# Kernel tuning notes

Hardware: AMD Instinct MI355X
Metric: run time of the kernel (lower is better)

## Reference

```python
import jax, jax.numpy as jnp
import numpy as np

N, M, D_IN, H1, D, OUT_C = 2048, 128, 352, 512, 256, 13


def _lin_bn_relu(x, w, b, g, be):
    # 1x1 conv == linear over last dim; BN (eval) folded to per-channel affine (g, be)
    return jax.nn.relu(g * (x @ w.T + b) + be)


def _encode(x, wA, bA, gA, beA, wB, bB, gB, beB):
    return _lin_bn_relu(_lin_bn_relu(x, wA, bA, gA, beA), wB, bB, gB, beB)


def setup_inputs() -> dict:
    key = jax.random.key(0)
    ks = iter(jax.random.split(key, 64))

    def wgt(shape, s=0.05):
        return (jax.random.normal(next(ks), shape, jnp.float32) * s)

    def gamma(c):
        return 1.0 + 0.05 * jax.random.normal(next(ks), (c,), jnp.float32)

    inp = {}
    inp['ext_fea'] = jax.random.normal(next(ks), (N, D_IN), jnp.float32)
    inp['lab_fea'] = jax.random.normal(next(ks), (M, D_IN), jnp.float32)
    # convs1: 352->512->256, each Conv1d(1x1)+BN+ReLU
    inp.update(w1a=wgt((H1, D_IN)), b1a=wgt((H1,)), g1a=gamma(H1), be1a=wgt((H1,)))
    inp.update(w1b=wgt((D, H1)), b1b=wgt((D,)), g1b=gamma(D), be1b=wgt((D,)))
    # convs2: same shapes
    inp.update(w2a=wgt((H1, D_IN)), b2a=wgt((H1,)), g2a=gamma(H1), be2a=wgt((H1,)))
    inp.update(w2b=wgt((D, H1)), b2b=wgt((D,)), g2b=gamma(D), be2b=wgt((D,)))
    # wei_conv SharedMLP [256,32,64,256]: three Conv2d(1x1)+BN+ReLU
    inp.update(mw1=wgt((32, D)), mb1=wgt((32,)), mg1=gamma(32), mbe1=wgt((32,)))
    inp.update(mw2=wgt((64, 32)), mb2=wgt((64,)), mg2=gamma(64), mbe2=wgt((64,)))
    inp.update(mw3=wgt((D, 64)), mb3=wgt((D,)), mg3=gamma(D), mbe3=wgt((D,)))
    # fc
    inp.update(fcw=wgt((OUT_C, D)), fcb=wgt((OUT_C,)))
    return inp


def reference(ext_fea, lab_fea,
              w1a, b1a, g1a, be1a, w1b, b1b, g1b, be1b,
              w2a, b2a, g2a, be2a, w2b, b2b, g2b, be2b,
              mw1, mb1, mg1, mbe1, mw2, mb2, mg2, mbe2, mw3, mb3, mg3, mbe3,
              fcw, fcb):
    A = _encode(ext_fea, w1a, b1a, g1a, be1a, w1b, b1b, g1b, be1b)   # [N, 256]
    B = _encode(lab_fea, w2a, b2a, g2a, be2a, w2b, b2b, g2b, be2b)   # [M, 256]
    diff = A[:, None, :] - B[None, :, :]                             # [N, M, 256]
    h = _lin_bn_relu(diff, mw1, mb1, mg1, mbe1)                      # [N, M, 32]
    h = _lin_bn_relu(h, mw2, mb2, mg2, mbe2)                         # [N, M, 64]
    wei = _lin_bn_relu(h, mw3, mb3, mg3, mbe3)                       # [N, M, 256]
    # torch softmax over dim=-1 of [1,256,N,M] == over M == axis 1 here
    wei = jax.nn.softmax(wei, axis=1)
    att = jnp.sum(wei * diff, axis=1)                                # [N, 256]
    return att @ fcw.T + fcb                                         # [N, 13]
```

## Files before the change

kernel.cpp:

```cpp
#include <hip/hip_runtime.h>
#include <stdint.h>


typedef __attribute__((ext_vector_type(4))) float float4_t;
typedef __attribute__((ext_vector_type(4))) float f32x4;
typedef __attribute__((ext_vector_type(8))) short bf16x8;
typedef __attribute__((ext_vector_type(8))) unsigned short ushort8_t;
typedef unsigned short ushort_t;

__device__ __forceinline__ unsigned short f2b(float f) {
  union { float f; unsigned int i; } v; v.f = f;
  unsigned int x = v.i;
  return (unsigned short)((x + 0x7FFFu + ((x >> 16) & 1u)) >> 16);
}

template<int ISBF>
__device__ __forceinline__ ushort8_t ld8(const void* base, size_t idx) {
  if constexpr (ISBF) {
    return *(const ushort8_t*)((const ushort_t*)base + idx);
  } else {
    const float* p = (const float*)base + idx;
    float4_t v0 = *(const float4_t*)p;
    float4_t v1 = *(const float4_t*)(p + 4);
    ushort8_t u;
    #pragma unroll
    for (int e = 0; e < 4; ++e) { u[e] = f2b(v0[e]); u[4 + e] = f2b(v1[e]); }
    return u;
  }
}

template<int XBF, int WBF, int OUT_BF16>
__global__ __launch_bounds__(256) void enc_mfma(
    const void* __restrict__ XA, const void* __restrict__ WA,
    const float* __restrict__ bA, const float* __restrict__ gA, const float* __restrict__ beA,
    void* __restrict__ YA,
    const void* __restrict__ XB, const void* __restrict__ WB,
    const float* __restrict__ bB, const float* __restrict__ gB, const float* __restrict__ beB,
    void* __restrict__ YB, float* __restrict__ YBT,
    int J, int K, int nbxA)
{
  __shared__ ushort_t Xs[64][40];
  __shared__ ushort_t Ws[64][40];
  const int bx = blockIdx.x, by = blockIdx.y;
  const void* X; const void* W;
  const float *bb, *gg, *bev; void* Y; int i0, isB;
  if (bx < nbxA) { X = XA; W = WA; bb = bA; gg = gA; bev = beA; Y = YA; i0 = bx * 64; isB = 0; }
  else           { X = XB; W = WB; bb = bB; gg = gB; bev = beB; Y = YB; i0 = (bx - nbxA) * 64; isB = 1; }
  const int j0 = by * 64;
  const int tid = threadIdx.x, w = tid >> 6, lane = tid & 63, lg = lane >> 4, lr = lane & 15;
  const int sr = tid >> 2, sk = (tid & 3) * 8;

  f32x4 acc[4];
  #pragma unroll
  for (int mt = 0; mt < 4; ++mt) acc[mt] = f32x4{0.f, 0.f, 0.f, 0.f};

  ushort8_t xv = ld8<XBF>(X, (size_t)(i0 + sr) * K + sk);
  ushort8_t wv = ld8<WBF>(W, (size_t)(j0 + sr) * K + sk);
  for (int kt = 0; kt < K; kt += 32) {
    __syncthreads();
    *(ushort8_t*)&Xs[sr][sk] = xv;
    *(ushort8_t*)&Ws[sr][sk] = wv;
    __syncthreads();
    if (kt + 32 < K) {
      xv = ld8<XBF>(X, (size_t)(i0 + sr) * K + kt + 32 + sk);
      wv = ld8<WBF>(W, (size_t)(j0 + sr) * K + kt + 32 + sk);
    }
    bf16x8 bfrag = *(const bf16x8*)&Ws[w * 16 + lr][lg * 8];
    #pragma unroll
    for (int mt = 0; mt < 4; ++mt) {
      bf16x8 af = *(const bf16x8*)&Xs[mt * 16 + lr][lg * 8];
      acc[mt] = __builtin_amdgcn_mfma_f32_16x16x32_bf16(af, bfrag, acc[mt], 0, 0, 0);
    }
  }
  const int c = j0 + w * 16 + lr;
  const float g = gg[c], bv = bb[c], ev = bev[c];
  #pragma unroll
  for (int mt = 0; mt < 4; ++mt)
    #pragma unroll
    for (int r = 0; r < 4; ++r) {
      const int row = i0 + mt * 16 + 4 * lg + r;
      float t = fmaxf(g * (acc[mt][r] + bv) + ev, 0.f);
      if (OUT_BF16) ((ushort_t*)Y)[(size_t)row * J + c] = f2b(t);
      else {
        ((float*)Y)[(size_t)row * J + c] = t;
        if (isB && YBT) YBT[(size_t)c * 128 + row] = t;
      }
    }
}

__global__ __launch_bounds__(256) void proj32(
    const float* __restrict__ Aenc, const float* __restrict__ Benc,
    const float* __restrict__ mw1, const float* __restrict__ mb1,
    const float* __restrict__ mg1, const float* __restrict__ mbe1,
    float* __restrict__ PA2, float* __restrict__ PB2, int nbxA,
    const float* __restrict__ mw2, const float* __restrict__ mw3,
    ushort_t* __restrict__ mw2b, ushort_t* __restrict__ mw3b)
{
  const int tid = threadIdx.x, bx = blockIdx.x;
  if (bx >= nbxA + 16) {
    const int g = (bx - nbxA - 16) * 256 + tid;
    const float* s; ushort_t* d; int j;
    if (g < 256) { s = mw2; d = mw2b; j = g; }
    else         { s = mw3; d = mw3b; j = g - 256; }
    float4_t v0 = *(const float4_t*)&s[(size_t)j * 8];
    float4_t v1 = *(const float4_t*)&s[(size_t)j * 8 + 4];
    ushort8_t u;
    #pragma unroll
    for (int e = 0; e < 4; ++e) { u[e] = f2b(v0[e]); u[4 + e] = f2b(v1[e]); }
    *(ushort8_t*)&d[(size_t)j * 8] = u;
    return;
  }
  const float* X; float* P; int n0, wb;
  if (bx < nbxA) { X = Aenc; P = PA2; n0 = bx * 8; wb = 1; }
  else           { X = Benc; P = PB2; n0 = (bx - nbxA) * 8; wb = 0; }
  const int r = tid >> 5, k = tid & 31;
  const int n = n0 + r;
  const float* xp = &X[(size_t)n * 256];
  const float* wp = &mw1[k * 256];
  float s = 0.f;
  #pragma unroll 8
  for (int q = 0; q < 256; q += 4) {
    float4_t xv = *(const float4_t*)&xp[q];
    float4_t wv = *(const float4_t*)&wp[q];
    #pragma unroll
    for (int e = 0; e < 4; ++e) s = fmaf(xv[e], wv[e], s);
  }
  P[(size_t)n * 32 + k] = wb ? (mg1[k] * (s + mb1[k]) + mbe1[k]) : (mg1[k] * s);
}

__global__ __launch_bounds__(256, 2) void main_attn(
    const float* __restrict__ PA2, const float* __restrict__ PB2,
    const float* __restrict__ A, const float* __restrict__ BmT,
    const ushort_t* __restrict__ mw2b, const float* __restrict__ mb2,
    const float* __restrict__ mg2, const float* __restrict__ mbe2,
    const ushort_t* __restrict__ mw3b, const float* __restrict__ mb3,
    const float* __restrict__ mg3, const float* __restrict__ mbe3,
    const float* __restrict__ fcw, const float* __restrict__ fcb,
    float* __restrict__ outp)
{
  __shared__ __align__(16) char smem[18432];
  ushort_t* h2s = (ushort_t*)smem;
  float* attL = (float*)smem;
  float* part = (float*)(smem + 1024);

  const int tid = threadIdx.x;
  const int w = tid >> 6, lane = tid & 63, lg = lane >> 4, lr = lane & 15;
  const int n = blockIdx.x;
  const float LOG2E = 1.4426950408889634f;

  {
    f32x4 acc1[2][4];
    #pragma unroll
    for (int mt = 0; mt < 2; ++mt)
      #pragma unroll
      for (int jt = 0; jt < 4; ++jt) acc1[mt][jt] = f32x4{0.f, 0.f, 0.f, 0.f};
    bf16x8 a1[2], b1[4];
    {
      const float* pa = &PA2[(size_t)n * 32 + lg * 8];
      float4_t pa0 = *(const float4_t*)pa;
      float4_t pa1 = *(const float4_t*)(pa + 4);
      #pragma unroll
      for (int mt = 0; mt < 2; ++mt) {
        const int m = w * 32 + mt * 16 + lr;
        const float* pb = &PB2[(size_t)m * 32 + lg * 8];
        float4_t pb0 = *(const float4_t*)pb;
        float4_t pb1 = *(const float4_t*)(pb + 4);
        bf16x8 u;
        #pragma unroll
        for (int e = 0; e < 4; ++e) {
          u[e]     = (short)f2b(fmaxf(pa0[e] - pb0[e], 0.f));
          u[4 + e] = (short)f2b(fmaxf(pa1[e] - pb1[e], 0.f));
        }
        a1[mt] = u;
      }
    }
    #pragma unroll
    for (int jt = 0; jt < 4; ++jt)
      b1[jt] = *(const bf16x8*)&mw2b[(jt * 16 + lr) * 32 + lg * 8];
    #pragma unroll
    for (int mt = 0; mt < 2; ++mt)
      #pragma unroll
      for (int jt = 0; jt < 4; ++jt)
        acc1[mt][jt] = __builtin_amdgcn_mfma_f32_16x16x32_bf16(a1[mt], b1[jt], acc1[mt][jt], 0, 0, 0);
    #pragma unroll
    for (int jt = 0; jt < 4; ++jt) {
      const int j = jt * 16 + lr;
      const float g = mg2[j], bv = mb2[j], ev = mbe2[j];
      #pragma unroll
      for (int mt = 0; mt < 2; ++mt)
        #pragma unroll
        for (int r = 0; r < 4; ++r)
          h2s[(w * 32 + mt * 16 + 4 * lg + r) * 72 + jt * 16 + lr] =
              f2b(fmaxf(g * (acc1[mt][jt][r] + bv) + ev, 0.f));
    }
  }
  __syncthreads();

  float smv[4], wbv[4];
  #pragma unroll
  for (int cp = 0; cp < 2; ++cp) {
    f32x4 acc[8][2];
    #pragma unroll
    for (int mt = 0; mt < 8; ++mt) {
      acc[mt][0] = f32x4{0.f, 0.f, 0.f, 0.f};
      acc[mt][1] = f32x4{0.f, 0.f, 0.f, 0.f};
    }
    #pragma unroll
    for (int ks = 0; ks < 2; ++ks) {
      bf16x8 bfr[2];
      #pragma unroll
      for (int q = 0; q < 2; ++q) {
        const int c = w * 64 + (cp * 2 + q) * 16 + lr;
        bfr[q] = *(const bf16x8*)&mw3b[(size_t)c * 64 + ks * 32 + lg * 8];
      }
      #pragma unroll
      for (int mt = 0; mt < 8; ++mt) {
        bf16x8 af = *(const bf16x8*)&h2s[(mt * 16 + lr) * 72 + ks * 32 + lg * 8];
        acc[mt][0] = __builtin_amdgcn_mfma_f32_16x16x32_bf16(af, bfr[0], acc[mt][0], 0, 0, 0);
        acc[mt][1] = __builtin_amdgcn_mfma_f32_16x16x32_bf16(af, bfr[1], acc[mt][1], 0, 0, 0);
      }
    }
    #pragma unroll
    for (int q = 0; q < 2; ++q) {
      const int ct = cp * 2 + q;
      const int c = w * 64 + ct * 16 + lr;
      const float g = mg3[c], bv = mb3[c], ev = mbe3[c];
      const float gs = g * LOG2E;
      const float cs = (g * bv + ev) * LOG2E;
      f32x4 sm4 = f32x4{0.f, 0.f, 0.f, 0.f};
      f32x4 wb4 = f32x4{0.f, 0.f, 0.f, 0.f};
      #pragma unroll
      for (int mt = 0; mt < 8; ++mt) {
        float4_t bv4 = *(const float4_t*)&BmT[(size_t)c * 128 + mt * 16 + 4 * lg];
        #pragma unroll
        for (int r = 0; r < 4; ++r) {
          float t = fmaf(gs, acc[mt][q][r], cs);
          float p = exp2f(__builtin_amdgcn_fmed3f(t, 0.f, 80.f));
          sm4[r] += p;
          wb4[r] = fmaf(p, bv4[r], wb4[r]);
        }
      }
      smv[ct] = (sm4[0] + sm4[1]) + (sm4[2] + sm4[3]);
      wbv[ct] = (wb4[0] + wb4[1]) + (wb4[2] + wb4[3]);
    }
  }
  #pragma unroll
  for (int st = 16; st <= 32; st <<= 1) {
    #pragma unroll
    for (int ct = 0; ct < 4; ++ct) {
      smv[ct] += __shfl_xor(smv[ct], st, 64);
      wbv[ct] += __shfl_xor(wbv[ct], st, 64);
    }
  }

  __syncthreads();
  if (lg == 0) {
    #pragma unroll
    for (int ct = 0; ct < 4; ++ct) {
      const int c = w * 64 + ct * 16 + lr;
      attL[c] = A[(size_t)n * 256 + c] - wbv[ct] / smv[ct];
    }
  }
  __syncthreads();

  {
    const int o = tid >> 4, gp = tid & 15;
    if (o < 13) {
      float s = 0.f;
      #pragma unroll
      for (int i = 0; i < 4; ++i) {
        float4_t av = *(const float4_t*)&attL[gp * 16 + i * 4];
        float4_t wv = *(const float4_t*)&fcw[(size_t)o * 256 + gp * 16 + i * 4];
        #pragma unroll
        for (int e = 0; e < 4; ++e) s = fmaf(av[e], wv[e], s);
      }
      part[o * 16 + gp] = s;
    }
  }
  __syncthreads();
  if (tid < 13) {
    float s = fcb[tid];
    #pragma unroll
    for (int gp = 0; gp < 16; ++gp) s += part[tid * 16 + gp];
    outp[(size_t)n * 13 + tid] = s;
  }
}

extern "C" void kernel_launch(void* const* d_in, const int* in_sizes, int n_in,
                              void* d_out, int out_size, void* d_ws, size_t ws_size,
                              hipStream_t stream)
{
  const float* ext = (const float*)d_in[0];
  const float* lab = (const float*)d_in[1];
  const float* w1a = (const float*)d_in[2];
  const float* b1a = (const float*)d_in[3];
  const float* g1a = (const float*)d_in[4];
  const float* be1a= (const float*)d_in[5];
  const float* w1b = (const float*)d_in[6];
  const float* b1b = (const float*)d_in[7];
  const float* g1b = (const float*)d_in[8];
  const float* be1b= (const float*)d_in[9];
  const float* w2a = (const float*)d_in[10];
  const float* b2a = (const float*)d_in[11];
  const float* g2a = (const float*)d_in[12];
  const float* be2a= (const float*)d_in[13];
  const float* w2b = (const float*)d_in[14];
  const float* b2b = (const float*)d_in[15];
  const float* g2b = (const float*)d_in[16];
  const float* be2b= (const float*)d_in[17];
  const float* mw1 = (const float*)d_in[18];
  const float* mb1 = (const float*)d_in[19];
  const float* mg1 = (const float*)d_in[20];
  const float* mbe1= (const float*)d_in[21];
  const float* mw2 = (const float*)d_in[22];
  const float* mb2 = (const float*)d_in[23];
  const float* mg2 = (const float*)d_in[24];
  const float* mbe2= (const float*)d_in[25];
  const float* mw3 = (const float*)d_in[26];
  const float* mb3 = (const float*)d_in[27];
  const float* mg3 = (const float*)d_in[28];
  const float* mbe3= (const float*)d_in[29];
  const float* fcw = (const float*)d_in[30];
  const float* fcb = (const float*)d_in[31];

  char* ws = (char*)d_ws;
  ushort_t* Y1ab = (ushort_t*)(ws);
  float*    PA2  = (float*)(ws);
  float*    PB2  = (float*)(ws + 262144);
  float*    Aenc = (float*)(ws + (2u << 20));
  char* b5 = ws + (4u << 20);
  ushort_t* mw2b = (ushort_t*)(b5);
  ushort_t* mw3b = (ushort_t*)(b5 + 4096);
  ushort_t* Y1bb = (ushort_t*)(b5 + 36864);
  float*    Benc = (float*)(b5 + 167936);
  float*    BencT= (float*)(b5 + 299008);

  enc_mfma<0, 0, 1><<<dim3(34, 8), 256, 0, stream>>>(
      (const void*)ext, (const void*)w1a, b1a, g1a, be1a, (void*)Y1ab,
      (const void*)lab, (const void*)w2a, b2a, g2a, be2a, (void*)Y1bb,
      (float*)nullptr, 512, 352, 32);
  enc_mfma<1, 0, 0><<<dim3(34, 4), 256, 0, stream>>>(
      (const void*)Y1ab, (const void*)w1b, b1b, g1b, be1b, (void*)Aenc,
      (const void*)Y1bb, (const void*)w2b, b2b, g2b, be2b, (void*)Benc,
      BencT, 256, 512, 32);
  proj32<<<281, 256, 0, stream>>>(Aenc, Benc, mw1, mb1, mg1, mbe1, PA2, PB2, 256,
                                  mw2, mw3, mw2b, mw3b);
  main_attn<<<2048, 256, 0, stream>>>(PA2, PB2, Aenc, BencT,
                                      mw2b, mb2, mg2, mbe2, mw3b, mb3, mg3, mbe3,
                                      fcw, fcb, (float*)d_out);
}
```

Baseline: 98.90 us.

## Retile encoder GEMMs smaller, split proj32 K, and process two rows per attention block

The encoder GEMM tile shrinks from 64x64 to 32x32 with double-buffered LDS and one sync per k-step, which quadruples the block count for better CU fill. proj32 splits the 256-wide dot product across two thread halves and combines them through LDS, doubling its grid. main_attn now handles two n rows per block, hoists the BN constants into registers, reuses the fc weights across both rows, and raises launch bounds to 3 blocks per CU. Smaller tiles cut data reuse per block, and the larger LDS footprint and register limit in main_attn may cause spills or lower occupancy.

```diff
diff --git a/kernel.cpp b/kernel.cpp
--- a/kernel.cpp
+++ b/kernel.cpp
@@ -39,53 +39,46 @@
     void* __restrict__ YB, float* __restrict__ YBT,
     int J, int K, int nbxA)
 {
-  __shared__ ushort_t Xs[64][40];
-  __shared__ ushort_t Ws[64][40];
+  __shared__ ushort_t Xs[2][32][40];
+  __shared__ ushort_t Ws[2][32][40];
   const int bx = blockIdx.x, by = blockIdx.y;
   const void* X; const void* W;
   const float *bb, *gg, *bev; void* Y; int i0, isB;
-  if (bx < nbxA) { X = XA; W = WA; bb = bA; gg = gA; bev = beA; Y = YA; i0 = bx * 64; isB = 0; }
-  else           { X = XB; W = WB; bb = bB; gg = gB; bev = beB; Y = YB; i0 = (bx - nbxA) * 64; isB = 1; }
-  const int j0 = by * 64;
+  if (bx < nbxA) { X = XA; W = WA; bb = bA; gg = gA; bev = beA; Y = YA; i0 = bx * 32; isB = 0; }
+  else           { X = XB; W = WB; bb = bB; gg = gB; bev = beB; Y = YB; i0 = (bx - nbxA) * 32; isB = 1; }
+  const int j0 = by * 32;
   const int tid = threadIdx.x, w = tid >> 6, lane = tid & 63, lg = lane >> 4, lr = lane & 15;
-  const int sr = tid >> 2, sk = (tid & 3) * 8;
-
-  f32x4 acc[4];
-  #pragma unroll
-  for (int mt = 0; mt < 4; ++mt) acc[mt] = f32x4{0.f, 0.f, 0.f, 0.f};
-
-  ushort8_t xv = ld8<XBF>(X, (size_t)(i0 + sr) * K + sk);
-  ushort8_t wv = ld8<WBF>(W, (size_t)(j0 + sr) * K + sk);
+  const int mt = w >> 1, ct = w & 1;
+  const int row = tid >> 2, k8 = (tid & 3) * 8;
+
+  f32x4 acc = f32x4{0.f, 0.f, 0.f, 0.f};
+
+  ushort8_t sv = (row < 32) ? ld8<XBF>(X, (size_t)(i0 + row) * K + k8)
+                            : ld8<WBF>(W, (size_t)(j0 + row - 32) * K + k8);
   for (int kt = 0; kt < K; kt += 32) {
+    const int buf = (kt >> 5) & 1;
+    if (row < 32) *(ushort8_t*)&Xs[buf][row][k8] = sv;
+    else          *(ushort8_t*)&Ws[buf][row - 32][k8] = sv;
     __syncthreads();
-    *(ushort8_t*)&Xs[sr][sk] = xv;
-    *(ushort8_t*)&Ws[sr][sk] = wv;
-    __syncthreads();
-    if (kt + 32 < K) {
-      xv = ld8<XBF>(X, (size_t)(i0 + sr) * K + kt + 32 + sk);
-      wv = ld8<WBF>(W, (size_t)(j0 + sr) * K + kt + 32 + sk);
-    }
-    bf16x8 bfrag = *(const bf16x8*)&Ws[w * 16 + lr][lg * 8];
-    #pragma unroll
-    for (int mt = 0; mt < 4; ++mt) {
-      bf16x8 af = *(const bf16x8*)&Xs[mt * 16 + lr][lg * 8];
-      acc[mt] = __builtin_amdgcn_mfma_f32_16x16x32_bf16(af, bfrag, acc[mt], 0, 0, 0);
-    }
-  }
-  const int c = j0 + w * 16 + lr;
+    if (kt + 32 < K)
+      sv = (row < 32) ? ld8<XBF>(X, (size_t)(i0 + row) * K + kt + 32 + k8)
+                      : ld8<WBF>(W, (size_t)(j0 + row - 32) * K + kt + 32 + k8);
+    bf16x8 af = *(const bf16x8*)&Xs[buf][mt * 16 + lr][lg * 8];
+    bf16x8 bf_ = *(const bf16x8*)&Ws[buf][ct * 16 + lr][lg * 8];
+    acc = __builtin_amdgcn_mfma_f32_16x16x32_bf16(af, bf_, acc, 0, 0, 0);
+  }
+  const int c = j0 + ct * 16 + lr;
   const float g = gg[c], bv = bb[c], ev = bev[c];
   #pragma unroll
-  for (int mt = 0; mt < 4; ++mt)
-    #pragma unroll
-    for (int r = 0; r < 4; ++r) {
-      const int row = i0 + mt * 16 + 4 * lg + r;
-      float t = fmaxf(g * (acc[mt][r] + bv) + ev, 0.f);
-      if (OUT_BF16) ((ushort_t*)Y)[(size_t)row * J + c] = f2b(t);
-      else {
-        ((float*)Y)[(size_t)row * J + c] = t;
-        if (isB && YBT) YBT[(size_t)c * 128 + row] = t;
-      }
-    }
+  for (int r = 0; r < 4; ++r) {
+    const int rowo = i0 + mt * 16 + 4 * lg + r;
+    float t = fmaxf(g * (acc[r] + bv) + ev, 0.f);
+    if (OUT_BF16) ((ushort_t*)Y)[(size_t)rowo * J + c] = f2b(t);
+    else {
+      ((float*)Y)[(size_t)rowo * J + c] = t;
+      if (isB && YBT) YBT[(size_t)c * 128 + rowo] = t;
+    }
+  }
 }
 
 __global__ __launch_bounds__(256) void proj32(
@@ -96,9 +89,10 @@
     const float* __restrict__ mw2, const float* __restrict__ mw3,
     ushort_t* __restrict__ mw2b, ushort_t* __restrict__ mw3b)
 {
+  __shared__ float ps[4][32];
   const int tid = threadIdx.x, bx = blockIdx.x;
-  if (bx >= nbxA + 16) {
-    const int g = (bx - nbxA - 16) * 256 + tid;
+  if (bx >= nbxA + 32) {
+    const int g = (bx - nbxA - 32) * 256 + tid;
     const float* s; ushort_t* d; int j;
     if (g < 256) { s = mw2; d = mw2b; j = g; }
     else         { s = mw3; d = mw3b; j = g - 256; }
@@ -111,24 +105,29 @@
     return;
   }
   const float* X; float* P; int n0, wb;
-  if (bx < nbxA) { X = Aenc; P = PA2; n0 = bx * 8; wb = 1; }
-  else           { X = Benc; P = PB2; n0 = (bx - nbxA) * 8; wb = 0; }
-  const int r = tid >> 5, k = tid & 31;
+  if (bx < nbxA) { X = Aenc; P = PA2; n0 = bx * 4; wb = 1; }
+  else           { X = Benc; P = PB2; n0 = (bx - nbxA) * 4; wb = 0; }
+  const int k = tid & 31, r = (tid >> 5) & 3, half = tid >> 7;
   const int n = n0 + r;
-  const float* xp = &X[(size_t)n * 256];
-  const float* wp = &mw1[k * 256];
+  const float* xp = &X[(size_t)n * 256 + half * 128];
+  const float* wp = &mw1[k * 256 + half * 128];
   float s = 0.f;
   #pragma unroll 8
-  for (int q = 0; q < 256; q += 4) {
+  for (int q = 0; q < 128; q += 4) {
     float4_t xv = *(const float4_t*)&xp[q];
     float4_t wv = *(const float4_t*)&wp[q];
     #pragma unroll
     for (int e = 0; e < 4; ++e) s = fmaf(xv[e], wv[e], s);
   }
-  P[(size_t)n * 32 + k] = wb ? (mg1[k] * (s + mb1[k]) + mbe1[k]) : (mg1[k] * s);
-}
-
-__global__ __launch_bounds__(256, 2) void main_attn(
+  if (half == 1) ps[r][k] = s;
+  __syncthreads();
+  if (half == 0) {
+    s += ps[r][k];
+    P[(size_t)n * 32 + k] = wb ? (mg1[k] * (s + mb1[k]) + mbe1[k]) : (mg1[k] * s);
+  }
+}
+
+__global__ __launch_bounds__(256, 3) void main_attn(
     const float* __restrict__ PA2, const float* __restrict__ PB2,
     const float* __restrict__ A, const float* __restrict__ BmT,
     const ushort_t* __restrict__ mw2b, const float* __restrict__ mb2,
@@ -138,127 +137,140 @@
     const float* __restrict__ fcw, const float* __restrict__ fcb,
     float* __restrict__ outp)
 {
-  __shared__ __align__(16) char smem[18432];
-  ushort_t* h2s = (ushort_t*)smem;
-  float* attL = (float*)smem;
-  float* part = (float*)(smem + 1024);
+  __shared__ __align__(16) char smem[40576];
+  float* attLs = (float*)(smem + 36864);
+  float* part  = (float*)(smem + 38912);
 
   const int tid = threadIdx.x;
   const int w = tid >> 6, lane = tid & 63, lg = lane >> 4, lr = lane & 15;
-  const int n = blockIdx.x;
+  const int n0 = blockIdx.x * 2;
   const float LOG2E = 1.4426950408889634f;
 
-  {
-    f32x4 acc1[2][4];
-    #pragma unroll
-    for (int mt = 0; mt < 2; ++mt)
-      #pragma unroll
-      for (int jt = 0; jt < 4; ++jt) acc1[mt][jt] = f32x4{0.f, 0.f, 0.f, 0.f};
-    bf16x8 a1[2], b1[4];
+  float g2h[4], b2h[4], e2h[4];
+  #pragma unroll
+  for (int jt = 0; jt < 4; ++jt) {
+    const int j = jt * 16 + lr;
+    g2h[jt] = mg2[j]; b2h[jt] = mb2[j]; e2h[jt] = mbe2[j];
+  }
+  float gs3[4], cs3[4];
+  #pragma unroll
+  for (int ct = 0; ct < 4; ++ct) {
+    const int c = w * 64 + ct * 16 + lr;
+    const float g = mg3[c];
+    gs3[ct] = g * LOG2E;
+    cs3[ct] = (g * mb3[c] + mbe3[c]) * LOG2E;
+  }
+
+  #pragma unroll
+  for (int nn = 0; nn < 2; ++nn) {
+    const int n = n0 + nn;
+    ushort_t* h2s = (ushort_t*)(smem + nn * 18432);
+
     {
-      const float* pa = &PA2[(size_t)n * 32 + lg * 8];
-      float4_t pa0 = *(const float4_t*)pa;
-      float4_t pa1 = *(const float4_t*)(pa + 4);
-      #pragma unroll
-      for (int mt = 0; mt < 2; ++mt) {
-        const int m = w * 32 + mt * 16 + lr;
-        const float* pb = &PB2[(size_t)m * 32 + lg * 8];
-        float4_t pb0 = *(const float4_t*)pb;
-        float4_t pb1 = *(const float4_t*)(pb + 4);
-        bf16x8 u;
-        #pragma unroll
-        for (int e = 0; e < 4; ++e) {
-          u[e]     = (short)f2b(fmaxf(pa0[e] - pb0[e], 0.f));
-          u[4 + e] = (short)f2b(fmaxf(pa1[e] - pb1[e], 0.f));
-        }
-        a1[mt] = u;
-      }
-    }
-    #pragma unroll
-    for (int jt = 0; jt < 4; ++jt)
-      b1[jt] = *(const bf16x8*)&mw2b[(jt * 16 + lr) * 32 + lg * 8];
-    #pragma unroll
-    for (int mt = 0; mt < 2; ++mt)
+      f32x4 acc1[2][4];
+      #pragma unroll
+      for (int mt = 0; mt < 2; ++mt)
+        #pragma unroll
+        for (int jt = 0; jt < 4; ++jt) acc1[mt][jt] = f32x4{0.f, 0.f, 0.f, 0.f};
+      bf16x8 a1[2], b1[4];
+      {
+        const float* pa = &PA2[(size_t)n * 32 + lg * 8];
+        float4_t pa0 = *(const float4_t*)pa;
+        float4_t pa1 = *(const float4_t*)(pa + 4);
+        #pragma unroll
+        for (int mt = 0; mt < 2; ++mt) {
+          const int m = w * 32 + mt * 16 + lr;
+          const float* pb = &PB2[(size_t)m * 32 + lg * 8];
+          float4_t pb0 = *(const float4_t*)pb;
+          float4_t pb1 = *(const float4_t*)(pb + 4);
+          bf16x8 u;
+          #pragma unroll
+          for (int e = 0; e < 4; ++e) {
+            u[e]     = (short)f2b(fmaxf(pa0[e] - pb0[e], 0.f));
+            u[4 + e] = (short)f2b(fmaxf(pa1[e] - pb1[e], 0.f));
+          }
+          a1[mt] = u;
+        }
+      }
       #pragma unroll
       for (int jt = 0; jt < 4; ++jt)
-        acc1[mt][jt] = __builtin_amdgcn_mfma_f32_16x16x32_bf16(a1[mt], b1[jt], acc1[mt][jt], 0, 0, 0);
-    #pragma unroll
-    for (int jt = 0; jt < 4; ++jt) {
-      const int j = jt * 16 + lr;
-      const float g = mg2[j], bv = mb2[j], ev = mbe2[j];
+        b1[jt] = *(const bf16x8*)&mw2b[(jt * 16 + lr) * 32 + lg * 8];
       #pragma unroll
       for (int mt = 0; mt < 2; ++mt)
         #pragma unroll
-        for (int r = 0; r < 4; ++r)
-          h2s[(w * 32 + mt * 16 + 4 * lg + r) * 72 + jt * 16 + lr] =
-              f2b(fmaxf(g * (acc1[mt][jt][r] + bv) + ev, 0.f));
-    }
-  }
-  __syncthreads();
-
-  float smv[4], wbv[4];
-  #pragma unroll
-  for (int cp = 0; cp < 2; ++cp) {
-    f32x4 acc[8][2];
-    #pragma unroll
-    for (int mt = 0; mt < 8; ++mt) {
-      acc[mt][0] = f32x4{0.f, 0.f, 0.f, 0.f};
-      acc[mt][1] = f32x4{0.f, 0.f, 0.f, 0.f};
-    }
-    #pragma unroll
-    for (int ks = 0; ks < 2; ++ks) {
-      bf16x8 bfr[2];
+        for (int jt = 0; jt < 4; ++jt)
+          acc1[mt][jt] = __builtin_amdgcn_mfma_f32_16x16x32_bf16(a1[mt], b1[jt], acc1[mt][jt], 0, 0, 0);
+      #pragma unroll
+      for (int jt = 0; jt < 4; ++jt) {
+        #pragma unroll
+        for (int mt = 0; mt < 2; ++mt)
+          #pragma unroll
+          for (int r = 0; r < 4; ++r)
+            h2s[(w * 32 + mt * 16 + 4 * lg + r) * 72 + jt * 16 + lr] =
+                f2b(fmaxf(g2h[jt] * (acc1[mt][jt][r] + b2h[jt]) + e2h[jt], 0.f));
+      }
+    }
+    __syncthreads();
+
+    float smv[4], wbv[4];
+    #pragma unroll
+    for (int cp = 0; cp < 2; ++cp) {
+      f32x4 acc[8][2];
+      #pragma unroll
+      for (int mt = 0; mt < 8; ++mt) {
+        acc[mt][0] = f32x4{0.f, 0.f, 0.f, 0.f};
+        acc[mt][1] = f32x4{0.f, 0.f, 0.f, 0.f};
+      }
+      #pragma unroll
+      for (int ks = 0; ks < 2; ++ks) {
+        bf16x8 bfr[2];
+        #pragma unroll
+        for (int q = 0; q < 2; ++q) {
+          const int c = w * 64 + (cp * 2 + q) * 16 + lr;
+          bfr[q] = *(const bf16x8*)&mw3b[(size_t)c * 64 + ks * 32 + lg * 8];
+        }
+        #pragma unroll
+        for (int mt = 0; mt < 8; ++mt) {
+          bf16x8 af = *(const bf16x8*)&h2s[(mt * 16 + lr) * 72 + ks * 32 + lg * 8];
+          acc[mt][0] = __builtin_amdgcn_mfma_f32_16x16x32_bf16(af, bfr[0], acc[mt][0], 0, 0, 0);
+          acc[mt][1] = __builtin_amdgcn_mfma_f32_16x16x32_bf16(af, bfr[1], acc[mt][1], 0, 0, 0);
+        }
+      }
       #pragma unroll
       for (int q = 0; q < 2; ++q) {
-        const int c = w * 64 + (cp * 2 + q) * 16 + lr;
-        bfr[q] = *(const bf16x8*)&mw3b[(size_t)c * 64 + ks * 32 + lg * 8];
-      }
-      #pragma unroll
-      for (int mt = 0; mt < 8; ++mt) {
-        bf16x8 af = *(const bf16x8*)&h2s[(mt * 16 + lr) * 72 + ks * 32 + lg * 8];
-        acc[mt][0] = __builtin_amdgcn_mfma_f32_16x16x32_bf16(af, bfr[0], acc[mt][0], 0, 0, 0);
-        acc[mt][1] = __builtin_amdgcn_mfma_f32_16x16x32_bf16(af, bfr[1], acc[mt][1], 0, 0, 0);
-      }
-    }
-    #pragma unroll
-    for (int q = 0; q < 2; ++q) {
-      const int ct = cp * 2 + q;
-      const int c = w * 64 + ct * 16 + lr;
-      const float g = mg3[c], bv = mb3[c], ev = mbe3[c];
-      const float gs = g * LOG2E;
-      const float cs = (g * bv + ev) * LOG2E;
-      f32x4 sm4 = f32x4{0.f, 0.f, 0.f, 0.f};
-      f32x4 wb4 = f32x4{0.f, 0.f, 0.f, 0.f};
-      #pragma unroll
-      for (int mt = 0; mt < 8; ++mt) {
-        float4_t bv4 = *(const float4_t*)&BmT[(size_t)c * 128 + mt * 16 + 4 * lg];
-        #pragma unroll
-        for (int r = 0; r < 4; ++r) {
-          float t = fmaf(gs, acc[mt][q][r], cs);
-          float p = exp2f(__builtin_amdgcn_fmed3f(t, 0.f, 80.f));
-          sm4[r] += p;
-          wb4[r] = fmaf(p, bv4[r], wb4[r]);
-        }
-      }
-      smv[ct] = (sm4[0] + sm4[1]) + (sm4[2] + sm4[3]);
-      wbv[ct] = (wb4[0] + wb4[1]) + (wb4[2] + wb4[3]);
-    }
-  }
-  #pragma unroll
-  for (int st = 16; st <= 32; st <<= 1) {
-    #pragma unroll
-    for (int ct = 0; ct < 4; ++ct) {
-      smv[ct] += __shfl_xor(smv[ct], st, 64);
-      wbv[ct] += __shfl_xor(wbv[ct], st, 64);
-    }
-  }
-
-  __syncthreads();
-  if (lg == 0) {
-    #pragma unroll
-    for (int ct = 0; ct < 4; ++ct) {
-      const int c = w * 64 + ct * 16 + lr;
-      attL[c] = A[(size_t)n * 256 + c] - wbv[ct] / smv[ct];
+        const int ct = cp * 2 + q;
+        const int c = w * 64 + ct * 16 + lr;
+        f32x4 sm4 = f32x4{0.f, 0.f, 0.f, 0.f};
+        f32x4 wb4 = f32x4{0.f, 0.f, 0.f, 0.f};
+        #pragma unroll
+        for (int mt = 0; mt < 8; ++mt) {
+          float4_t bv4 = *(const float4_t*)&BmT[(size_t)c * 128 + mt * 16 + 4 * lg];
+          #pragma unroll
+          for (int r = 0; r < 4; ++r) {
+            float t = fmaf(gs3[ct], acc[mt][q][r], cs3[ct]);
+            float p = exp2f(__builtin_amdgcn_fmed3f(t, 0.f, 80.f));
+            sm4[r] += p;
+            wb4[r] = fmaf(p, bv4[r], wb4[r]);
+          }
+        }
+        smv[ct] = (sm4[0] + sm4[1]) + (sm4[2] + sm4[3]);
+        wbv[ct] = (wb4[0] + wb4[1]) + (wb4[2] + wb4[3]);
+      }
+    }
+    #pragma unroll
+    for (int st = 16; st <= 32; st <<= 1) {
+      #pragma unroll
+      for (int ct = 0; ct < 4; ++ct) {
+        smv[ct] += __shfl_xor(smv[ct], st, 64);
+        wbv[ct] += __shfl_xor(wbv[ct], st, 64);
+      }
+    }
+    if (lg == 0) {
+      #pragma unroll
+      for (int ct = 0; ct < 4; ++ct) {
+        const int c = w * 64 + ct * 16 + lr;
+        attLs[nn * 256 + c] = A[(size_t)n * 256 + c] - wbv[ct] / smv[ct];
+      }
     }
   }
   __syncthreads();
@@ -266,23 +278,30 @@
   {
     const int o = tid >> 4, gp = tid & 15;
     if (o < 13) {
-      float s = 0.f;
-      #pragma unroll
-      for (int i = 0; i < 4; ++i) {
-        float4_t av = *(const float4_t*)&attL[gp * 16 + i * 4];
-        float4_t wv = *(const float4_t*)&fcw[(size_t)o * 256 + gp * 16 + i * 4];
-        #pragma unroll
-        for (int e = 0; e < 4; ++e) s = fmaf(av[e], wv[e], s);
-      }
-      part[o * 16 + gp] = s;
+      float4_t wv[4];
+      #pragma unroll
+      for (int i = 0; i < 4; ++i)
+        wv[i] = *(const float4_t*)&fcw[(size_t)o * 256 + gp * 16 + i * 4];
+      #pragma unroll
+      for (int nn = 0; nn < 2; ++nn) {
+        float s = 0.f;
+        #pragma unroll
+        for (int i = 0; i < 4; ++i) {
+          float4_t av = *(const float4_t*)&attLs[nn * 256 + gp * 16 + i * 4];
+          #pragma unroll
+          for (int e = 0; e < 4; ++e) s = fmaf(av[e], wv[i][e], s);
+        }
+        part[nn * 208 + o * 16 + gp] = s;
+      }
     }
   }
   __syncthreads();
-  if (tid < 13) {
-    float s = fcb[tid];
-    #pragma unroll
-    for (int gp = 0; gp < 16; ++gp) s += part[tid * 16 + gp];
-    outp[(size_t)n * 13 + tid] = s;
+  if (tid < 26) {
+    const int nn = tid / 13, o = tid % 13;
+    float s = fcb[o];
+    #pragma unroll
+    for (int gp = 0; gp < 16; ++gp) s += part[nn * 208 + o * 16 + gp];
+    outp[(size_t)(n0 + nn) * 13 + o] = s;
   }
 }
 
@@ -335,17 +354,17 @@
   float*    Benc = (float*)(b5 + 167936);
   float*    BencT= (float*)(b5 + 299008);
 
-  enc_mfma<0, 0, 1><<<dim3(34, 8), 256, 0, stream>>>(
+  enc_mfma<0, 0, 1><<<dim3(68, 16), 256, 0, stream>>>(
       (const void*)ext, (const void*)w1a, b1a, g1a, be1a, (void*)Y1ab,
       (const void*)lab, (const void*)w2a, b2a, g2a, be2a, (void*)Y1bb,
-      (float*)nullptr, 512, 352, 32);
-  enc_mfma<1, 0, 0><<<dim3(34, 4), 256, 0, stream>>>(
+      (float*)nullptr, 512, 352, 64);
+  enc_mfma<1, 0, 0><<<dim3(68, 8), 256, 0, stream>>>(
       (const void*)Y1ab, (const void*)w1b, b1b, g1b, be1b, (void*)Aenc,
       (const void*)Y1bb, (const void*)w2b, b2b, g2b, be2b, (void*)Benc,
-      BencT, 256, 512, 32);
-  proj32<<<281, 256, 0, stream>>>(Aenc, Benc, mw1, mb1, mg1, mbe1, PA2, PB2, 256,
+      BencT, 256, 512, 64);
+  proj32<<<553, 256, 0, stream>>>(Aenc, Benc, mw1, mb1, mg1, mbe1, PA2, PB2, 512,
                                   mw2, mw3, mw2b, mw3b);
-  main_attn<<<2048, 256, 0, stream>>>(PA2, PB2, Aenc, BencT,
+  main_attn<<<1024, 256, 0, stream>>>(PA2, PB2, Aenc, BencT,
                                       mw2b, mb2, mg2, mbe2, mw3b, mb3, mg3, mbe3,
                                       fcw, fcb, (float*)d_out);
 }
```

Result: slower. 125.2 us (+26.6%).
